# Kernel optimization log

Measured on AMD Instinct MI355X. Metric: run time of the kernel, lower is better.

The kernel has to match this reference:

```python
import jax, jax.numpy as jnp
import numpy as np

# dims
L, D, N, H, FF, F = 2, 512, 8, 64, 2048, 256   # layers, embed, heads, head_dim, ffn, feature_dim
BQ, BC, TQ, TC = 8, 32, 128, 128               # query batch, candidate batch, tokens
EPS = 1e-6


def setup_inputs() -> dict:
    key = jax.random.key(0)
    ks = iter(jax.random.split(key, 64))
    nrm = lambda shape, s=0.02: jax.random.normal(next(ks), shape, jnp.float32) * s
    inp = {
        "c": jax.random.normal(next(ks), (BC, TC, D), jnp.float32),
        "q": jax.random.normal(next(ks), (BQ, TQ, D), jnp.float32),
    }
    for p in ("sa", "ca"):  # self-attn / cross-attn per decoder layer, stacked over L
        inp[f"{p}_wq"] = nrm((L, D, N, H)); inp[f"{p}_bq"] = nrm((L, N, 1, H))
        inp[f"{p}_wk"] = nrm((L, D, N, H)); inp[f"{p}_bk"] = nrm((L, N, 1, H))
        inp[f"{p}_wv"] = nrm((L, D, N, H)); inp[f"{p}_bv"] = nrm((L, N, 1, H))
        inp[f"{p}_wo"] = nrm((L, N, D, H)); inp[f"{p}_bo"] = nrm((L, D))
    for i in (1, 2, 3):  # post-norm LayerNorms
        inp[f"ln{i}_g"] = jnp.ones((L, D), jnp.float32)
        inp[f"ln{i}_b"] = jnp.zeros((L, D), jnp.float32)
    inp["ffn_w1"] = nrm((L, D, FF)); inp["ffn_b1"] = jnp.zeros((L, FF), jnp.float32)
    inp["ffn_w2"] = nrm((L, FF, D)); inp["ffn_b2"] = jnp.zeros((L, D), jnp.float32)
    inp["lnf_g"] = jnp.ones((D,), jnp.float32); inp["lnf_b"] = jnp.zeros((D,), jnp.float32)
    inp["feat_wq"] = nrm((D, F)); inp["feat_bq"] = jnp.zeros((F,), jnp.float32)
    inp["feat_wc"] = nrm((D, F)); inp["feat_bc"] = jnp.zeros((F,), jnp.float32)
    return inp


def _ln(x, g, b):
    m = x.mean(-1, keepdims=True)
    v = ((x - m) ** 2).mean(-1, keepdims=True)
    return (x - m) * jax.lax.rsqrt(v + EPS) * g + b


def _mha4d(xq, xkv, wq, bq, wk, bk, wv, bv, wo, bo):
    # query reads axes as (e,b), key/value as (b,e): the swapped leading axes make
    # the matmul broadcast queries against candidates when e/b are singleton.
    Q = jnp.einsum('ebtd,dnh->ebnth', xq, wq) + bq   # [e,b,n,t,h]
    K = jnp.einsum('betd,dnh->benth', xkv, wk) + bk  # [b,e,n,s,h]
    V = jnp.einsum('betd,dnh->benth', xkv, wv) + bv
    scores = jnp.matmul(Q, jnp.swapaxes(K, -1, -2)) / np.sqrt(H)  # broadcast -> [B,E,n,t,s]
    A = jax.nn.softmax(scores, axis=-1)
    O = jnp.matmul(A, V)                              # [B,E,n,t,h]
    return jnp.einsum('benth,ndh->betd', O, wo) + bo  # [B,E,t,d]


def reference(c, q, sa_wq, sa_bq, sa_wk, sa_bk, sa_wv, sa_bv, sa_wo, sa_bo,
              ca_wq, ca_bq, ca_wk, ca_bk, ca_wv, ca_bv, ca_wo, ca_bo,
              ln1_g, ln1_b, ln2_g, ln2_b, ln3_g, ln3_b,
              ffn_w1, ffn_b1, ffn_w2, ffn_b2, lnf_g, lnf_b,
              feat_wq, feat_bq, feat_wc, feat_bc):
    qm = q[:, None]   # [BQ,1,TQ,D]  encoder memory
    x = c[None]       # [1,BC,TC,D]  decoder input
    for i in range(L):
        a = _mha4d(x, x, sa_wq[i], sa_bq[i], sa_wk[i], sa_bk[i], sa_wv[i], sa_bv[i], sa_wo[i], sa_bo[i])
        x = _ln(x + a, ln1_g[i], ln1_b[i])
        a = _mha4d(x, qm, ca_wq[i], ca_bq[i], ca_wk[i], ca_bk[i], ca_wv[i], ca_bv[i], ca_wo[i], ca_bo[i])
        x = _ln(x + a, ln2_g[i], ln2_b[i])  # x: [BQ,BC,TC,D]
        h = jax.nn.relu(x @ ffn_w1[i] + ffn_b1[i]) @ ffn_w2[i] + ffn_b2[i]
        x = _ln(x + h, ln3_g[i], ln3_b[i])
    x = _ln(x, lnf_g, lnf_b)
    # pooling='avg': drop token 0 then mean over token axis (axis=2)
    qp = qm[:, :, 1:, :].mean(axis=2)  # [BQ,1,D]
    cp = x[:, :, 1:, :].mean(axis=2)   # [BQ,BC,D]
    qf = qp @ feat_wq + feat_bq        # [BQ,1,F]
    cf = cp @ feat_wc + feat_bc        # [BQ,BC,F]
    qn = qf * jax.lax.rsqrt(jnp.maximum((qf ** 2).sum(-1, keepdims=True), 1e-12))
    cn = cf * jax.lax.rsqrt(jnp.maximum((cf ** 2).sum(-1, keepdims=True), 1e-12))
    return (qn * cn).sum(-1)           # [BQ,BC] cosine similarity
```

## Files before the change

### kernel.cpp

```cpp
#include <hip/hip_runtime.h>

using half4  = __attribute__((ext_vector_type(4))) _Float16;
using half8  = __attribute__((ext_vector_type(8))) _Float16;
using floatx4 = __attribute__((ext_vector_type(4))) float;

__device__ __forceinline__ void gl_lds16(const _Float16* g, _Float16* l)
{
  __builtin_amdgcn_global_load_lds(
      (const __attribute__((address_space(1))) void*)g,
      (__attribute__((address_space(3))) void*)l, 16, 0, 0);
}

__global__ __launch_bounds__(256) void gemm_h(
    const _Float16* __restrict__ A, const _Float16* __restrict__ Bt,
    const float* __restrict__ bias, _Float16* __restrict__ C,
    int M, int N, int K, int ldC, int relu)
{
  __shared__ _Float16 As[128 * 32];
  __shared__ _Float16 Bs[128 * 32];
  int tid = threadIdx.x;
  int lane = tid & 63, wave = tid >> 6;
  long bm0 = (long)blockIdx.y * 128;
  int bn0 = blockIdx.x * 128;
  int wm = (wave & 1) * 64, wn = (wave >> 1) * 64;
  int srow = wave * 16 + (lane >> 2);
  int scol = (((lane & 3) ^ ((lane >> 3) & 3)) * 8);
  const _Float16* aA0 = A + (bm0 + srow) * (long)K + scol;
  const _Float16* aA1 = aA0 + 64 * (long)K;
  const _Float16* aB0 = Bt + (bn0 + srow) * (long)K + scol;
  const _Float16* aB1 = aB0 + 64 * (long)K;
  _Float16* lA0 = As + wave * 512;
  _Float16* lA1 = As + 2048 + wave * 512;
  _Float16* lB0 = Bs + wave * 512;
  _Float16* lB1 = Bs + 2048 + wave * 512;
  int mrow = lane & 15, quad = lane >> 4;
  int cofs = (quad ^ ((mrow >> 1) & 3)) * 8;
  floatx4 acc[4][4];
#pragma unroll
  for (int i = 0; i < 4; ++i)
#pragma unroll
    for (int j = 0; j < 4; ++j) acc[i][j] = (floatx4){0.f, 0.f, 0.f, 0.f};

  for (int kt = 0; kt < K; kt += 32) {
    __syncthreads();
    gl_lds16(aA0 + kt, lA0);
    gl_lds16(aA1 + kt, lA1);
    gl_lds16(aB0 + kt, lB0);
    gl_lds16(aB1 + kt, lB1);
    __syncthreads();
    half8 af[4], bf[4];
#pragma unroll
    for (int i = 0; i < 4; ++i)
      af[i] = *(const half8*)&As[(wm + 16 * i + mrow) * 32 + cofs];
#pragma unroll
    for (int j = 0; j < 4; ++j)
      bf[j] = *(const half8*)&Bs[(wn + 16 * j + mrow) * 32 + cofs];
#pragma unroll
    for (int i = 0; i < 4; ++i)
#pragma unroll
      for (int j = 0; j < 4; ++j)
        acc[i][j] = __builtin_amdgcn_mfma_f32_16x16x32_f16(af[i], bf[j], acc[i][j], 0, 0, 0);
  }
#pragma unroll
  for (int j = 0; j < 4; ++j) {
    int n = bn0 + wn + 16 * j + mrow;
    float bj = bias[n];
#pragma unroll
    for (int i = 0; i < 4; ++i) {
#pragma unroll
      for (int r = 0; r < 4; ++r) {
        long m = bm0 + wm + 16 * i + quad * 4 + r;
        float v = acc[i][j][r] + bj;
        if (relu) v = fmaxf(v, 0.f);
        C[m * (long)ldC + n] = (_Float16)v;
      }
    }
  }
}

__global__ __launch_bounds__(256, 2) void gemm_2(
    const _Float16* __restrict__ A, const _Float16* __restrict__ Bt,
    const float* __restrict__ bias, _Float16* __restrict__ C,
    int MT, int NT, int K, int ldC, int relu)
{
  __shared__ _Float16 As[256 * 64];
  __shared__ _Float16 Bs[128 * 64];
  int tid = threadIdx.x;
  int lane = tid & 63, wave = tid >> 6;
  int L = blockIdx.x;
  int xcd = L & 7, seq = L >> 3;
  int band = MT >> 3;
  int mt = xcd * band + seq / NT;
  int nt = seq - (seq / NT) * NT;
  long bm0 = (long)mt * 256;
  int bn0 = nt * 128;
  int r8 = lane >> 3, s8 = lane & 7;
  int scol = (s8 ^ r8) * 8;
  const _Float16* aA = A + (bm0 + wave * 64 + r8) * (long)K + scol;
  const _Float16* aB = Bt + (bn0 + wave * 32 + r8) * (long)K + scol;
  _Float16* lA = As + (wave * 64) * 64;
  _Float16* lB = Bs + (wave * 32) * 64;
  int ll = lane & 15, quad = lane >> 4;
  int lw = ll & 7;
  floatx4 acc[4][8];
#pragma unroll
  for (int i = 0; i < 4; ++i)
#pragma unroll
    for (int j = 0; j < 8; ++j) acc[i][j] = (floatx4){0.f, 0.f, 0.f, 0.f};

  for (int kt = 0; kt < K; kt += 64) {
    __syncthreads();
#pragma unroll
    for (int o = 0; o < 8; ++o)
      gl_lds16(aA + (long)(o * 8) * K + kt, lA + o * 512);
#pragma unroll
    for (int o = 0; o < 4; ++o)
      gl_lds16(aB + (long)(o * 8) * K + kt, lB + o * 512);
    __syncthreads();
#pragma unroll
    for (int k2 = 0; k2 < 2; ++k2) {
      int sofs = ((k2 * 4 + quad) ^ lw) * 8;
      half8 af[4], bf[8];
#pragma unroll
      for (int i = 0; i < 4; ++i)
        af[i] = *(const half8*)&As[(wave * 64 + 16 * i + ll) * 64 + sofs];
#pragma unroll
      for (int j = 0; j < 8; ++j)
        bf[j] = *(const half8*)&Bs[(16 * j + ll) * 64 + sofs];
#pragma unroll
      for (int i = 0; i < 4; ++i)
#pragma unroll
        for (int j = 0; j < 8; ++j)
          acc[i][j] = __builtin_amdgcn_mfma_f32_16x16x32_f16(af[i], bf[j], acc[i][j], 0, 0, 0);
    }
  }
#pragma unroll
  for (int j = 0; j < 8; ++j) {
    int n = bn0 + 16 * j + ll;
    float bj = bias[n];
#pragma unroll
    for (int i = 0; i < 4; ++i) {
#pragma unroll
      for (int r = 0; r < 4; ++r) {
        long m = bm0 + wave * 64 + 16 * i + quad * 4 + r;
        float v = acc[i][j][r] + bj;
        if (relu) v = fmaxf(v, 0.f);
        C[m * (long)ldC + n] = (_Float16)v;
      }
    }
  }
}

__global__ __launch_bounds__(256) void attn_h(
    const _Float16* __restrict__ Qp, int qs,
    const _Float16* __restrict__ Kp, const _Float16* __restrict__ Vp, int ks,
    _Float16* __restrict__ Op, int mode_ca, int l0, int rb0)
{
  __shared__ _Float16 KV[128 * 72];
  __shared__ _Float16 Ps[128 * 136];
  int tid = threadIdx.x;
  int lane = tid & 63, wave = tid >> 6;
  int ll = lane & 15, quad = lane >> 4;
  int idx = blockIdx.x;
  int n = idx & 7;
  int rl = idx >> 3;
  long obase = (long)rl * 128 * 512 + n * 64;
  long qoff, koff;
  if (!mode_ca) {
    qoff = (long)rl * 128 * qs + n * 64;
    koff = (long)rl * 128 * ks + n * 64;
  } else {
    int g = rb0 + rl;
    int a = g >> 5;
    int qblk = l0 ? (g & 31) : rl;
    qoff = (long)qblk * 128 * qs + n * 64;
    koff = (long)a * 128 * ks + n * 64;
  }
#pragma unroll
  for (int it = 0; it < 4; ++it) {
    int e = tid + it * 256;
    int r = e >> 3, c = (e & 7) * 8;
    *(half8*)&KV[r * 72 + c] = *(const half8*)&Kp[koff + (long)r * ks + c];
  }
  half8 aQ[2][2];
#pragma unroll
  for (int i = 0; i < 2; ++i)
#pragma unroll
    for (int k2 = 0; k2 < 2; ++k2)
      aQ[i][k2] = *(const half8*)&Qp[qoff + (long)(wave * 32 + i * 16 + ll) * qs
                                     + quad * 8 + k2 * 32];
  half8 vreg[4];
#pragma unroll
  for (int it = 0; it < 4; ++it) {
    int e = tid + it * 256;
    int vr = e >> 3, c = (e & 7) * 8;
    vreg[it] = *(const half8*)&Vp[koff + (long)vr * ks + c];
  }
  __syncthreads();
  floatx4 accS[2][8];
#pragma unroll
  for (int i = 0; i < 2; ++i)
#pragma unroll
    for (int j = 0; j < 8; ++j) accS[i][j] = (floatx4){0.f, 0.f, 0.f, 0.f};
#pragma unroll
  for (int k2 = 0; k2 < 2; ++k2) {
#pragma unroll
    for (int j = 0; j < 8; ++j) {
      half8 bK = *(const half8*)&KV[(j * 16 + ll) * 72 + quad * 8 + k2 * 32];
      accS[0][j] = __builtin_amdgcn_mfma_f32_16x16x32_f16(aQ[0][k2], bK, accS[0][j], 0, 0, 0);
      accS[1][j] = __builtin_amdgcn_mfma_f32_16x16x32_f16(aQ[1][k2], bK, accS[1][j], 0, 0, 0);
    }
  }
  float rinv[2][4];
#pragma unroll
  for (int i = 0; i < 2; ++i) {
#pragma unroll
    for (int r = 0; r < 4; ++r) {
      float mx = -1e30f;
#pragma unroll
      for (int j = 0; j < 8; ++j) {
        accS[i][j][r] *= 0.125f;
        mx = fmaxf(mx, accS[i][j][r]);
      }
#pragma unroll
      for (int off = 1; off < 16; off <<= 1) mx = fmaxf(mx, __shfl_xor(mx, off));
      float s = 0.f;
#pragma unroll
      for (int j = 0; j < 8; ++j) {
        float e = __expf(accS[i][j][r] - mx);
        accS[i][j][r] = e;
        s += e;
      }
#pragma unroll
      for (int off = 1; off < 16; off <<= 1) s += __shfl_xor(s, off);
      rinv[i][r] = 1.f / s;
      int prow = wave * 32 + i * 16 + quad * 4 + r;
#pragma unroll
      for (int j = 0; j < 8; ++j)
        Ps[prow * 136 + j * 16 + ll] = (_Float16)accS[i][j][r];
    }
  }
  __syncthreads();
#pragma unroll
  for (int it = 0; it < 4; ++it) {
    int e = tid + it * 256;
    int vr = e >> 3, c = (e & 7) * 8;
#pragma unroll
    for (int j = 0; j < 8; ++j) KV[(c + j) * 132 + vr] = vreg[it][j];
  }
  __syncthreads();
  floatx4 accO[2][4];
#pragma unroll
  for (int i = 0; i < 2; ++i)
#pragma unroll
    for (int j = 0; j < 4; ++j) accO[i][j] = (floatx4){0.f, 0.f, 0.f, 0.f};
#pragma unroll
  for (int k4 = 0; k4 < 4; ++k4) {
    half8 aP[2];
#pragma unroll
    for (int i = 0; i < 2; ++i)
      aP[i] = *(const half8*)&Ps[(wave * 32 + i * 16 + ll) * 136 + quad * 8 + k4 * 32];
#pragma unroll
    for (int jh = 0; jh < 4; ++jh) {
      int vb = (jh * 16 + ll) * 132 + quad * 8 + k4 * 32;
      half4 v0 = *(const half4*)&KV[vb];
      half4 v1 = *(const half4*)&KV[vb + 4];
      half8 bV = __builtin_shufflevector(v0, v1, 0, 1, 2, 3, 4, 5, 6, 7);
      accO[0][jh] = __builtin_amdgcn_mfma_f32_16x16x32_f16(aP[0], bV, accO[0][jh], 0, 0, 0);
      accO[1][jh] = __builtin_amdgcn_mfma_f32_16x16x32_f16(aP[1], bV, accO[1][jh], 0, 0, 0);
    }
  }
#pragma unroll
  for (int i = 0; i < 2; ++i)
#pragma unroll
    for (int jh = 0; jh < 4; ++jh)
#pragma unroll
      for (int r = 0; r < 4; ++r) {
        int m = wave * 32 + i * 16 + quad * 4 + r;
        Op[obase + (long)m * 512 + jh * 16 + ll] = (_Float16)(accO[i][jh][r] * rinv[i][r]);
      }
}

__global__ __launch_bounds__(256) void ln_h(
    const void* __restrict__ xin, int xf32, const _Float16* __restrict__ add,
    _Float16* __restrict__ out, const float* __restrict__ g,
    const float* __restrict__ bt, long row0, int bmask)
{
  int rl = blockIdx.x * 4 + (threadIdx.x >> 6);
  long row = row0 + rl;
  int lane = threadIdx.x & 63;
  long xr = (row & (long)bmask) * 512 + lane * 8;
  float v[8];
  if (xf32) {
    float4 a0 = *(const float4*)((const float*)xin + xr);
    float4 a1 = *(const float4*)((const float*)xin + xr + 4);
    v[0] = a0.x; v[1] = a0.y; v[2] = a0.z; v[3] = a0.w;
    v[4] = a1.x; v[5] = a1.y; v[6] = a1.z; v[7] = a1.w;
  } else {
    half8 h = *(const half8*)((const _Float16*)xin + xr);
#pragma unroll
    for (int i = 0; i < 8; ++i) v[i] = (float)h[i];
  }
  if (add) {
    half8 a = *(const half8*)&add[(long)rl * 512 + lane * 8];
#pragma unroll
    for (int i = 0; i < 8; ++i) v[i] += (float)a[i];
  }
  float s = 0.f, sq = 0.f;
#pragma unroll
  for (int i = 0; i < 8; ++i) { s += v[i]; sq += v[i] * v[i]; }
#pragma unroll
  for (int off = 1; off < 64; off <<= 1) {
    s += __shfl_xor(s, off);
    sq += __shfl_xor(sq, off);
  }
  float mean = s * (1.f / 512.f);
  float var = sq * (1.f / 512.f) - mean * mean;
  float rst = rsqrtf(var + 1e-6f);
  int c = lane * 8;
  float4 g0 = *(const float4*)&g[c], g1 = *(const float4*)&g[c + 4];
  float4 b0 = *(const float4*)&bt[c], b1 = *(const float4*)&bt[c + 4];
  float gg[8] = {g0.x, g0.y, g0.z, g0.w, g1.x, g1.y, g1.z, g1.w};
  float bb[8] = {b0.x, b0.y, b0.z, b0.w, b1.x, b1.y, b1.z, b1.w};
  half8 o;
#pragma unroll
  for (int i = 0; i < 8; ++i) o[i] = (_Float16)((v[i] - mean) * rst * gg[i] + bb[i]);
  *(half8*)&out[row * 512 + c] = o;
}

__global__ __launch_bounds__(256) void tconv512(
    const float* __restrict__ w0, const float* __restrict__ w1,
    const float* __restrict__ w2, const float* __restrict__ w3,
    const float* __restrict__ w4, const float* __restrict__ w5,
    _Float16* __restrict__ Wh)
{
  __shared__ float T[64][65];
  int z = blockIdx.z;
  int t = z >> 1, l = z & 1;
  const float* src;
  long off;
  switch (t) {
    case 0: src = w0; off = 0; break;
    case 1: src = w1; off = 262144; break;
    case 2: src = w2; off = 524288; break;
    case 3: src = w3; off = 1048576; break;
    case 4: src = w4; off = 1310720; break;
    default: src = w5; off = 1572864; break;
  }
  src += (long)l * 262144;
  _Float16* out = Wh + (long)l * 4194304 + off;
  int tx = threadIdx.x & 63, tg = threadIdx.x >> 6;
  int r0 = blockIdx.y * 64, c0 = blockIdx.x * 64;
#pragma unroll
  for (int i = 0; i < 16; ++i)
    T[tg + 4 * i][tx] = src[(long)(r0 + tg + 4 * i) * 512 + c0 + tx];
  __syncthreads();
#pragma unroll
  for (int i = 0; i < 16; ++i)
    out[(long)(c0 + tg + 4 * i) * 512 + r0 + tx] = (_Float16)T[tx][tg + 4 * i];
}

__global__ __launch_bounds__(256) void tconvL(const float* __restrict__ in,
                                              _Float16* __restrict__ out, int Rr, int Cc,
                                              long ils, long ols)
{
  __shared__ float T[64][65];
  in += (long)blockIdx.z * ils;
  out += (long)blockIdx.z * ols;
  int tx = threadIdx.x & 63, tg = threadIdx.x >> 6;
  int r0 = blockIdx.y * 64, c0 = blockIdx.x * 64;
#pragma unroll
  for (int i = 0; i < 16; ++i)
    T[tg + 4 * i][tx] = in[(long)(r0 + tg + 4 * i) * Cc + c0 + tx];
  __syncthreads();
#pragma unroll
  for (int i = 0; i < 16; ++i)
    out[(long)(c0 + tg + 4 * i) * Rr + r0 + tx] = (_Float16)T[tx][tg + 4 * i];
}

__global__ void woconvB(const float* __restrict__ sa_wo, const float* __restrict__ ca_wo,
                        _Float16* __restrict__ Wh)
{
  int z = blockIdx.y;
  int s = z >> 1, l = z & 1;
  const float* wo = (s ? ca_wo : sa_wo) + (long)l * 262144;
  _Float16* out = Wh + (long)l * 4194304 + (s ? 1835008 : 786432);
  int o = blockIdx.x * 256 + threadIdx.x;
  int d = o >> 9;
  int nh = o & 511;
  int n = nh >> 6, h = nh & 63;
  out[o] = (_Float16)wo[((long)(n << 9) + d) * 64 + h];
}

__global__ void packbias(const float* __restrict__ sa_bq, const float* __restrict__ sa_bk,
                         const float* __restrict__ sa_bv, const float* __restrict__ ca_bk,
                         const float* __restrict__ ca_bv, float* __restrict__ Bqkv,
                         float* __restrict__ Bkv)
{
  int i = blockIdx.x * 256 + threadIdx.x;
  if (i >= 5120) return;
  int reg = i >> 9, idx = i & 511;
  int l = reg / 5, r = reg % 5;
  int lo = l * 512;
  switch (r) {
    case 0: Bqkv[l * 1536 + idx] = sa_bq[lo + idx]; break;
    case 1: Bqkv[l * 1536 + 512 + idx] = sa_bk[lo + idx]; break;
    case 2: Bqkv[l * 1536 + 1024 + idx] = sa_bv[lo + idx]; break;
    case 3: Bkv[l * 1024 + idx] = ca_bk[lo + idx]; break;
    default: Bkv[l * 1024 + 512 + idx] = ca_bv[lo + idx]; break;
  }
}

__global__ void f2h2(const float* __restrict__ a, _Float16* __restrict__ oa, long na,
                     const float* __restrict__ bsrc, _Float16* __restrict__ ob, long nb)
{
  long i = blockIdx.x * 256L + threadIdx.x;
  if (i < na) oa[i] = (_Float16)a[i];
  else if (i < na + nb) ob[i - na] = (_Float16)bsrc[i - na];
}

__global__ void featq_pool(const float* __restrict__ q, const float* __restrict__ W,
                           const float* __restrict__ bias, float* __restrict__ QN)
{
  __shared__ float sh[512];
  __shared__ float red[256];
  int a = blockIdx.x;
  int f = threadIdx.x;
  for (int dd = f; dd < 512; dd += 256) {
    const float* base = q + (long)a * 65536 + dd;
    float s = 0.f;
    for (int t = 1; t < 128; ++t) s += base[t * 512];
    sh[dd] = s * (1.f / 127.f);
  }
  __syncthreads();
  float acc = bias[f];
  for (int d = 0; d < 512; ++d) acc += sh[d] * W[d * 256 + f];
  red[f] = acc * acc;
  __syncthreads();
  for (int s = 128; s > 0; s >>= 1) {
    if (f < s) red[f] += red[f + s];
    __syncthreads();
  }
  float rn = rsqrtf(fmaxf(red[0], 1e-12f));
  QN[a * 256 + f] = acc * rn;
}

__global__ void featc_pool(const _Float16* __restrict__ X, const float* __restrict__ W,
                           const float* __restrict__ bias, const float* __restrict__ QN,
                           float* __restrict__ out)
{
  __shared__ float sh[512];
  __shared__ float red[256];
  int ab = blockIdx.x;
  int f = threadIdx.x;
  for (int dd = f; dd < 512; dd += 256) {
    const _Float16* base = X + (long)ab * 65536 + dd;
    float s = 0.f;
    for (int t = 1; t < 128; ++t) s += (float)base[t * 512];
    sh[dd] = s * (1.f / 127.f);
  }
  __syncthreads();
  float acc = bias[f];
  for (int d = 0; d < 512; ++d) acc += sh[d] * W[d * 256 + f];
  red[f] = acc * acc;
  __syncthreads();
  for (int s = 128; s > 0; s >>= 1) {
    if (f < s) red[f] += red[f + s];
    __syncthreads();
  }
  float rn = rsqrtf(fmaxf(red[0], 1e-12f));
  float v = acc * rn * QN[(ab >> 5) * 256 + f];
  __syncthreads();
  red[f] = v;
  __syncthreads();
  for (int s = 128; s > 0; s >>= 1) {
    if (f < s) red[f] += red[f + s];
    __syncthreads();
  }
  if (f == 0) out[ab] = red[0];
}

extern "C" void kernel_launch(void* const* d_in, const int* in_sizes, int n_in,
                              void* d_out, int out_size, void* d_ws, size_t ws_size,
                              hipStream_t stream)
{
  (void)in_sizes; (void)n_in; (void)out_size;
  const float* c_in  = (const float*)d_in[0];
  const float* q_in  = (const float*)d_in[1];
  const float* sa_wq = (const float*)d_in[2];
  const float* sa_bq = (const float*)d_in[3];
  const float* sa_wk = (const float*)d_in[4];
  const float* sa_bk = (const float*)d_in[5];
  const float* sa_wv = (const float*)d_in[6];
  const float* sa_bv = (const float*)d_in[7];
  const float* sa_wo = (const float*)d_in[8];
  const float* sa_bo = (const float*)d_in[9];
  const float* ca_wq = (const float*)d_in[10];
  const float* ca_bq = (const float*)d_in[11];
  const float* ca_wk = (const float*)d_in[12];
  const float* ca_bk = (const float*)d_in[13];
  const float* ca_wv = (const float*)d_in[14];
  const float* ca_bv = (const float*)d_in[15];
  const float* ca_wo = (const float*)d_in[16];
  const float* ca_bo = (const float*)d_in[17];
  const float* ln1_g = (const float*)d_in[18];
  const float* ln1_b = (const float*)d_in[19];
  const float* ln2_g = (const float*)d_in[20];
  const float* ln2_b = (const float*)d_in[21];
  const float* ln3_g = (const float*)d_in[22];
  const float* ln3_b = (const float*)d_in[23];
  const float* ffn_w1 = (const float*)d_in[24];
  const float* ffn_b1 = (const float*)d_in[25];
  const float* ffn_w2 = (const float*)d_in[26];
  const float* ffn_b2 = (const float*)d_in[27];
  const float* lnf_g  = (const float*)d_in[28];
  const float* lnf_b  = (const float*)d_in[29];
  const float* feat_wq = (const float*)d_in[30];
  const float* feat_bq = (const float*)d_in[31];
  const float* feat_wc = (const float*)d_in[32];
  const float* feat_bc = (const float*)d_in[33];

  char* p = (char*)d_ws;
  _Float16* Xh  = (_Float16*)p;  p += 33554432;
  _Float16* Xsh = (_Float16*)p;  p += 4194304;
  _Float16* Wh  = (_Float16*)p;  p += 16777216;
  _Float16* qh  = (_Float16*)p;  p += 1048576;
  _Float16* KV0 = (_Float16*)p;  p += 2097152;
  float*    Bqkv = (float*)p;    p += 12288;
  float*    Bkv  = (float*)p;    p += 8192;
  float*    QN  = (float*)p;     p += 8192;
  const size_t fixed_b = (size_t)(p - (char*)d_ws);
  long R = 4096;
  if (ws_size >= fixed_b + 5120UL * 32768) R = 32768;
  else if (ws_size >= fixed_b + 5120UL * 16384) R = 16384;
  else if (ws_size >= fixed_b + 5120UL * 8192) R = 8192;
  _Float16* QKVc = (_Float16*)p; p += R * 3072;
  _Float16* Oc   = (_Float16*)p; p += R * 1024;
  _Float16* Ac   = (_Float16*)p;
  _Float16* Hb = QKVc;
  const int MTR = (int)(R / 256);

  f2h2<<<10240, 256, 0, stream>>>(c_in, Xsh, 2097152, q_in, qh, 524288);
  tconv512<<<dim3(8, 8, 12), 256, 0, stream>>>(sa_wq, sa_wk, sa_wv, ca_wq, ca_wk, ca_wv, Wh);
  woconvB<<<dim3(1024, 4), 256, 0, stream>>>(sa_wo, ca_wo, Wh);
  tconvL<<<dim3(32, 8, 2), 256, 0, stream>>>(ffn_w1, Wh + 2097152, 512, 2048, 1048576, 4194304);
  tconvL<<<dim3(8, 32, 2), 256, 0, stream>>>(ffn_w2, Wh + 3145728, 2048, 512, 1048576, 4194304);
  packbias<<<20, 256, 0, stream>>>(sa_bq, sa_bk, sa_bv, ca_bk, ca_bv, Bqkv, Bkv);

  {
    _Float16* Wl = Wh;
    gemm_h<<<dim3(12, 32), 256, 0, stream>>>(Xsh, Wl + 0, Bqkv, QKVc, 4096, 1536, 512, 1536, 0);
    attn_h<<<256, 256, 0, stream>>>(QKVc, 1536, QKVc + 512, QKVc + 1024, 1536, Oc, 0, 0, 0);
    gemm_h<<<dim3(4, 32), 256, 0, stream>>>(Oc, Wl + 786432, sa_bo, Ac, 4096, 512, 512, 512, 0);
    ln_h<<<1024, 256, 0, stream>>>(c_in, 1, Ac, Xsh, ln1_g, ln1_b, 0, 0x7FFFFFFF);
    gemm_h<<<dim3(4, 32), 256, 0, stream>>>(Xsh, Wl + 1048576, ca_bq, QKVc, 4096, 512, 512, 1536, 0);
    gemm_h<<<dim3(8, 8), 256, 0, stream>>>(qh, Wl + 1310720, Bkv, KV0, 1024, 1024, 512, 1024, 0);
    for (long c = 0; c < 32768; c += R) {
      attn_h<<<(R / 128) * 8, 256, 0, stream>>>(QKVc, 1536, KV0, KV0 + 512, 1024, Oc,
                                                1, 1, (int)(c / 128));
      gemm_2<<<MTR * 4, 256, 0, stream>>>(Oc, Wl + 1835008, ca_bo, Ac, MTR, 4, 512, 512, 0);
      ln_h<<<R / 4, 256, 0, stream>>>(Xsh, 0, Ac, Xh, ln2_g, ln2_b, c, 4095);
      gemm_2<<<MTR * 16, 256, 0, stream>>>(Xh + c * 512, Wl + 2097152,
                                           ffn_b1, Hb, MTR, 16, 512, 2048, 1);
      gemm_2<<<MTR * 4, 256, 0, stream>>>(Hb, Wl + 3145728, ffn_b2, Ac, MTR, 4, 2048, 512, 0);
      ln_h<<<R / 4, 256, 0, stream>>>(Xh, 0, Ac, Xh, ln3_g, ln3_b, c, 0x7FFFFFFF);
    }
  }
  {
    _Float16* Wl = Wh + 4194304;
    gemm_h<<<dim3(8, 8), 256, 0, stream>>>(qh, Wl + 1310720, Bkv + 1024, KV0, 1024, 1024, 512, 1024, 0);
    for (long c = 0; c < 32768; c += R) {
      _Float16* Xhc = Xh + c * 512;
      gemm_2<<<MTR * 12, 256, 0, stream>>>(Xhc, Wl + 0, Bqkv + 1536, QKVc, MTR, 12, 512, 1536, 0);
      attn_h<<<(R / 128) * 8, 256, 0, stream>>>(QKVc, 1536, QKVc + 512, QKVc + 1024, 1536,
                                                Oc, 0, 0, 0);
      gemm_2<<<MTR * 4, 256, 0, stream>>>(Oc, Wl + 786432, sa_bo + 512, Ac, MTR, 4, 512, 512, 0);
      ln_h<<<R / 4, 256, 0, stream>>>(Xh, 0, Ac, Xh, ln1_g + 512, ln1_b + 512, c, 0x7FFFFFFF);
      gemm_2<<<MTR * 4, 256, 0, stream>>>(Xhc, Wl + 1048576, ca_bq + 512, QKVc, MTR, 4, 512, 1536, 0);
      attn_h<<<(R / 128) * 8, 256, 0, stream>>>(QKVc, 1536, KV0, KV0 + 512, 1024, Oc,
                                                1, 0, (int)(c / 128));
      gemm_2<<<MTR * 4, 256, 0, stream>>>(Oc, Wl + 1835008, ca_bo + 512, Ac, MTR, 4, 512, 512, 0);
      ln_h<<<R / 4, 256, 0, stream>>>(Xh, 0, Ac, Xh, ln2_g + 512, ln2_b + 512, c, 0x7FFFFFFF);
      gemm_2<<<MTR * 16, 256, 0, stream>>>(Xh + c * 512, Wl + 2097152,
                                           ffn_b1 + 2048, Hb, MTR, 16, 512, 2048, 1);
      gemm_2<<<MTR * 4, 256, 0, stream>>>(Hb, Wl + 3145728, ffn_b2 + 512, Ac, MTR, 4, 2048, 512, 0);
      ln_h<<<R / 4, 256, 0, stream>>>(Xh, 0, Ac, Xh, ln3_g + 512, ln3_b + 512, c, 0x7FFFFFFF);
    }
  }
  ln_h<<<8192, 256, 0, stream>>>(Xh, 0, nullptr, Xh, lnf_g, lnf_b, 0, 0x7FFFFFFF);
  featq_pool<<<8, 256, 0, stream>>>(q_in, feat_wq, feat_bq, QN);
  featc_pool<<<256, 256, 0, stream>>>(Xh, feat_wc, feat_bc, QN, (float*)d_out);
}
```

Before: 925.7 us.

## Double-buffer LDS in main GEMM with async prefetch and hand-scheduled reads

Replaces the single-buffered 256x128 GEMM kernel with a double-buffered one. It shrinks the K tile to 32 so two stages fit in the same 48KB of LDS, and prefetches the next K tile with global_load_lds while MFMAs consume the current one. LDS fragment reads are issued as inline-asm ds_read_b128 with immediate offsets, waits are explicit, and s_setprio is raised around the MFMA block. This aims to hide global-load latency and halve the barriers per K step. In exchange there are more loop iterations and a new swizzle to get right, and the hand-placed waitcnt/sched barriers can stall if misplaced.

```diff
diff --git a/kernel.cpp b/kernel.cpp
--- a/kernel.cpp
+++ b/kernel.cpp
@@ -10,6 +10,24 @@
       (const __attribute__((address_space(1))) void*)g,
       (__attribute__((address_space(3))) void*)l, 16, 0, 0);
 }
+
+__device__ __forceinline__ uint32_t lds_u32(const _Float16* p)
+{
+  return (uint32_t)(uintptr_t)(const __attribute__((address_space(3))) _Float16*)p;
+}
+
+template<int IMM>
+__device__ __forceinline__ half8 dsr(uint32_t addr)
+{
+  half8 r;
+  asm volatile("ds_read_b128 %0, %1 offset:%2" : "=v"(r) : "v"(addr), "i"(IMM));
+  return r;
+}
+
+#define LGK0() do { asm volatile("s_waitcnt lgkmcnt(0)" ::: "memory"); \
+                    __builtin_amdgcn_sched_barrier(0); } while (0)
+#define VM0()  do { asm volatile("s_waitcnt vmcnt(0)" ::: "memory"); \
+                    __builtin_amdgcn_sched_barrier(0); } while (0)
 
 __global__ __launch_bounds__(256) void gemm_h(
     const _Float16* __restrict__ A, const _Float16* __restrict__ Bt,
@@ -78,13 +96,12 @@
   }
 }
 
-__global__ __launch_bounds__(256, 2) void gemm_2(
+__global__ __launch_bounds__(256, 2) void gemm_d(
     const _Float16* __restrict__ A, const _Float16* __restrict__ Bt,
     const float* __restrict__ bias, _Float16* __restrict__ C,
     int MT, int NT, int K, int ldC, int relu)
 {
-  __shared__ _Float16 As[256 * 64];
-  __shared__ _Float16 Bs[128 * 64];
+  __shared__ _Float16 S[24576];
   int tid = threadIdx.x;
   int lane = tid & 63, wave = tid >> 6;
   int L = blockIdx.x;
@@ -94,49 +111,71 @@
   int nt = seq - (seq / NT) * NT;
   long bm0 = (long)mt * 256;
   int bn0 = nt * 128;
-  int r8 = lane >> 3, s8 = lane & 7;
-  int scol = (s8 ^ r8) * 8;
-  const _Float16* aA = A + (bm0 + wave * 64 + r8) * (long)K + scol;
-  const _Float16* aB = Bt + (bn0 + wave * 32 + r8) * (long)K + scol;
-  _Float16* lA = As + (wave * 64) * 64;
-  _Float16* lB = Bs + (wave * 32) * 64;
-  int ll = lane & 15, quad = lane >> 4;
-  int lw = ll & 7;
+  int srow = lane >> 2;
+  int scol = (((lane & 3) ^ ((lane >> 3) & 3)) * 8);
+  const _Float16* aA = A + (bm0 + wave * 64 + srow) * (long)K + scol;
+  const _Float16* aB = Bt + (bn0 + wave * 32 + srow) * (long)K + scol;
+  _Float16* lA = S + (wave * 64) * 32;
+  _Float16* lB = S + 8192 + (wave * 32) * 32;
+  int mrow = lane & 15, quad = lane >> 4;
+  int cofs = (quad ^ ((mrow >> 1) & 3)) * 8;
+  uint32_t abase = lds_u32(S) + (uint32_t)((wave * 64 + mrow) * 32 + cofs) * 2u;
+  uint32_t bbase = lds_u32(S) + 16384u + (uint32_t)(mrow * 32 + cofs) * 2u;
   floatx4 acc[4][8];
 #pragma unroll
   for (int i = 0; i < 4; ++i)
 #pragma unroll
     for (int j = 0; j < 8; ++j) acc[i][j] = (floatx4){0.f, 0.f, 0.f, 0.f};
 
-  for (int kt = 0; kt < K; kt += 64) {
-    __syncthreads();
-#pragma unroll
-    for (int o = 0; o < 8; ++o)
-      gl_lds16(aA + (long)(o * 8) * K + kt, lA + o * 512);
-#pragma unroll
-    for (int o = 0; o < 4; ++o)
-      gl_lds16(aB + (long)(o * 8) * K + kt, lB + o * 512);
-    __syncthreads();
-#pragma unroll
-    for (int k2 = 0; k2 < 2; ++k2) {
-      int sofs = ((k2 * 4 + quad) ^ lw) * 8;
-      half8 af[4], bf[8];
-#pragma unroll
-      for (int i = 0; i < 4; ++i)
-        af[i] = *(const half8*)&As[(wave * 64 + 16 * i + ll) * 64 + sofs];
+  int NTK = K >> 5;
+#pragma unroll
+  for (int o = 0; o < 4; ++o)
+    gl_lds16(aA + (long)(o * 16) * K, lA + o * 512);
+#pragma unroll
+  for (int o = 0; o < 2; ++o)
+    gl_lds16(aB + (long)(o * 16) * K, lB + o * 512);
+  VM0();
+  __builtin_amdgcn_s_barrier();
+
+  for (int t = 0; t < NTK; ++t) {
+    uint32_t db = (t & 1) ? 24576u : 0u;
+    __builtin_amdgcn_sched_barrier(0);
+    if (t + 1 < NTK) {
+      uint32_t nb = ((t + 1) & 1) ? 24576u : 0u;
+      _Float16* nA = S + nb / 2;
+      _Float16* nB = nA + 8192;
+      int kt = (t + 1) << 5;
+#pragma unroll
+      for (int o = 0; o < 4; ++o)
+        gl_lds16(aA + kt + (long)(o * 16) * K, nA + (wave * 64) * 32 + o * 512);
+#pragma unroll
+      for (int o = 0; o < 2; ++o)
+        gl_lds16(aB + kt + (long)(o * 16) * K, nB + (wave * 32) * 32 + o * 512);
+    }
+    __builtin_amdgcn_sched_barrier(0);
+    uint32_t a = abase + db, b = bbase + db;
+    half8 af[4], bf[8];
+    af[0] = dsr<0>(a);    af[1] = dsr<1024>(a);
+    af[2] = dsr<2048>(a); af[3] = dsr<3072>(a);
+    bf[0] = dsr<0>(b);    bf[1] = dsr<1024>(b);
+    bf[2] = dsr<2048>(b); bf[3] = dsr<3072>(b);
+    bf[4] = dsr<4096>(b); bf[5] = dsr<5120>(b);
+    bf[6] = dsr<6144>(b); bf[7] = dsr<7168>(b);
+    LGK0();
+    __builtin_amdgcn_s_setprio(1);
+#pragma unroll
+    for (int i = 0; i < 4; ++i)
 #pragma unroll
       for (int j = 0; j < 8; ++j)
-        bf[j] = *(const half8*)&Bs[(16 * j + ll) * 64 + sofs];
-#pragma unroll
-      for (int i = 0; i < 4; ++i)
-#pragma unroll
-        for (int j = 0; j < 8; ++j)
-          acc[i][j] = __builtin_amdgcn_mfma_f32_16x16x32_f16(af[i], bf[j], acc[i][j], 0, 0, 0);
-    }
+        acc[i][j] = __builtin_amdgcn_mfma_f32_16x16x32_f16(af[i], bf[j], acc[i][j], 0, 0, 0);
+    __builtin_amdgcn_s_setprio(0);
+    __builtin_amdgcn_sched_barrier(0);
+    VM0();
+    __builtin_amdgcn_s_barrier();
   }
 #pragma unroll
   for (int j = 0; j < 8; ++j) {
-    int n = bn0 + 16 * j + ll;
+    int n = bn0 + 16 * j + mrow;
     float bj = bias[n];
 #pragma unroll
     for (int i = 0; i < 4; ++i) {
@@ -558,11 +597,11 @@
     for (long c = 0; c < 32768; c += R) {
       attn_h<<<(R / 128) * 8, 256, 0, stream>>>(QKVc, 1536, KV0, KV0 + 512, 1024, Oc,
                                                 1, 1, (int)(c / 128));
-      gemm_2<<<MTR * 4, 256, 0, stream>>>(Oc, Wl + 1835008, ca_bo, Ac, MTR, 4, 512, 512, 0);
+      gemm_d<<<MTR * 4, 256, 0, stream>>>(Oc, Wl + 1835008, ca_bo, Ac, MTR, 4, 512, 512, 0);
       ln_h<<<R / 4, 256, 0, stream>>>(Xsh, 0, Ac, Xh, ln2_g, ln2_b, c, 4095);
-      gemm_2<<<MTR * 16, 256, 0, stream>>>(Xh + c * 512, Wl + 2097152,
+      gemm_d<<<MTR * 16, 256, 0, stream>>>(Xh + c * 512, Wl + 2097152,
                                            ffn_b1, Hb, MTR, 16, 512, 2048, 1);
-      gemm_2<<<MTR * 4, 256, 0, stream>>>(Hb, Wl + 3145728, ffn_b2, Ac, MTR, 4, 2048, 512, 0);
+      gemm_d<<<MTR * 4, 256, 0, stream>>>(Hb, Wl + 3145728, ffn_b2, Ac, MTR, 4, 2048, 512, 0);
       ln_h<<<R / 4, 256, 0, stream>>>(Xh, 0, Ac, Xh, ln3_g, ln3_b, c, 0x7FFFFFFF);
     }
   }
@@ -571,19 +610,19 @@
     gemm_h<<<dim3(8, 8), 256, 0, stream>>>(qh, Wl + 1310720, Bkv + 1024, KV0, 1024, 1024, 512, 1024, 0);
     for (long c = 0; c < 32768; c += R) {
       _Float16* Xhc = Xh + c * 512;
-      gemm_2<<<MTR * 12, 256, 0, stream>>>(Xhc, Wl + 0, Bqkv + 1536, QKVc, MTR, 12, 512, 1536, 0);
+      gemm_d<<<MTR * 12, 256, 0, stream>>>(Xhc, Wl + 0, Bqkv + 1536, QKVc, MTR, 12, 512, 1536, 0);
       attn_h<<<(R / 128) * 8, 256, 0, stream>>>(QKVc, 1536, QKVc + 512, QKVc + 1024, 1536,
                                                 Oc, 0, 0, 0);
-      gemm_2<<<MTR * 4, 256, 0, stream>>>(Oc, Wl + 786432, sa_bo + 512, Ac, MTR, 4, 512, 512, 0);
+      gemm_d<<<MTR * 4, 256, 0, stream>>>(Oc, Wl + 786432, sa_bo + 512, Ac, MTR, 4, 512, 512, 0);
       ln_h<<<R / 4, 256, 0, stream>>>(Xh, 0, Ac, Xh, ln1_g + 512, ln1_b + 512, c, 0x7FFFFFFF);
-      gemm_2<<<MTR * 4, 256, 0, stream>>>(Xhc, Wl + 1048576, ca_bq + 512, QKVc, MTR, 4, 512, 1536, 0);
+      gemm_d<<<MTR * 4, 256, 0, stream>>>(Xhc, Wl + 1048576, ca_bq + 512, QKVc, MTR, 4, 512, 1536, 0);
       attn_h<<<(R / 128) * 8, 256, 0, stream>>>(QKVc, 1536, KV0, KV0 + 512, 1024, Oc,
                                                 1, 0, (int)(c / 128));
-      gemm_2<<<MTR * 4, 256, 0, stream>>>(Oc, Wl + 1835008, ca_bo + 512, Ac, MTR, 4, 512, 512, 0);
+      gemm_d<<<MTR * 4, 256, 0, stream>>>(Oc, Wl + 1835008, ca_bo + 512, Ac, MTR, 4, 512, 512, 0);
       ln_h<<<R / 4, 256, 0, stream>>>(Xh, 0, Ac, Xh, ln2_g + 512, ln2_b + 512, c, 0x7FFFFFFF);
-      gemm_2<<<MTR * 16, 256, 0, stream>>>(Xh + c * 512, Wl + 2097152,
+      gemm_d<<<MTR * 16, 256, 0, stream>>>(Xh + c * 512, Wl + 2097152,
                                            ffn_b1 + 2048, Hb, MTR, 16, 512, 2048, 1);
-      gemm_2<<<MTR * 4, 256, 0, stream>>>(Hb, Wl + 3145728, ffn_b2 + 512, Ac, MTR, 4, 2048, 512, 0);
+      gemm_d<<<MTR * 4, 256, 0, stream>>>(Hb, Wl + 3145728, ffn_b2 + 512, Ac, MTR, 4, 2048, 512, 0);
       ln_h<<<R / 4, 256, 0, stream>>>(Xh, 0, Ac, Xh, ln3_g + 512, ln3_b + 512, c, 0x7FFFFFFF);
     }
   }
```

New measurement: 970.7 us. +4.9%, slower.
